# Kernel optimization log

Measured on AMD Instinct MI355X. Metric: run time of the kernel, lower is better.

Reference implementation:

```python
import jax, jax.numpy as jnp
import numpy as np

NUM_GLOBAL_EXPERTS = 256
LOCAL_START = 64  # global experts [64, 128) live on this rank


def setup_inputs() -> dict:
    key = jax.random.key(0)
    k1, = jax.random.split(key, 1)
    num_local_experts = 64
    # Routing ids: ~4.2M tokens x topk=8, values are GLOBAL expert ids in [0, 256)
    topk_ids = jax.random.randint(k1, (33554432,), 0, NUM_GLOBAL_EXPERTS, dtype=jnp.int32)
    # expert_map: global -> local; -1 for experts not owned by this rank
    gid = jnp.arange(NUM_GLOBAL_EXPERTS, dtype=jnp.int32)
    expert_map = jnp.where(
        (gid >= LOCAL_START) & (gid < LOCAL_START + num_local_experts),
        gid - LOCAL_START,
        jnp.int32(-1),
    )
    return {"topk_ids": topk_ids, "num_local_experts": num_local_experts, "expert_map": expert_map}


def reference(topk_ids, num_local_experts, expert_map=None):
    n = num_local_experts  # static python int
    ids = topk_ids.reshape(-1)
    if expert_map is not None:
        # invalid ids (< 0) stay invalid; valid global ids are remapped to local space
        ids = jnp.where(ids >= 0, expert_map[jnp.clip(ids, 0)], jnp.int32(-1))
    # Route all invalid / out-of-range ids into an overflow bucket n, then drop it.
    valid = (ids >= 0) & (ids < n)
    bucket = jnp.where(valid, ids, jnp.int32(n))
    counts = jax.ops.segment_sum(
        jnp.ones_like(bucket, dtype=jnp.int32), bucket, num_segments=n + 1
    )
    return counts[:n].astype(jnp.int32)
```

## Files before the change

### kernel.cpp

```cpp
#include <hip/hip_runtime.h>

#define BLOCK 256
#define NBLOCKS 1024
#define NBINS 256
#define NWAVES 4

__global__ __launch_bounds__(BLOCK) void hist_kernel(const int* __restrict__ ids,
                                                     int N,
                                                     const int* __restrict__ expert_map,
                                                     int* __restrict__ out,
                                                     int n_local) {
    __shared__ int lds[NWAVES * NBINS];
    const int tid = threadIdx.x;

    for (int i = tid; i < NWAVES * NBINS; i += BLOCK) lds[i] = 0;
    __syncthreads();

    int* h = &lds[(tid >> 6) * NBINS];

    const long long n4 = (long long)(N >> 2);
    const int4* __restrict__ ids4 = (const int4*)ids;
    const long long stride = (long long)gridDim.x * BLOCK;

    for (long long i = (long long)blockIdx.x * BLOCK + tid; i < n4; i += stride) {
        int4 v = ids4[i];
        atomicAdd(&h[v.x & (NBINS - 1)], 1);
        atomicAdd(&h[v.y & (NBINS - 1)], 1);
        atomicAdd(&h[v.z & (NBINS - 1)], 1);
        atomicAdd(&h[v.w & (NBINS - 1)], 1);
    }

    if (blockIdx.x == 0) {
        long long base = n4 << 2;
        for (long long i = base + tid; i < (long long)N; i += BLOCK) {
            atomicAdd(&h[ids[i] & (NBINS - 1)], 1);
        }
    }
    __syncthreads();

    if (tid < NBINS) {
        int sum = 0;
#pragma unroll
        for (int w = 0; w < NWAVES; ++w) sum += lds[w * NBINS + tid];
        int local = expert_map[tid];
        if (local >= 0 && local < n_local && sum > 0) {
            atomicAdd(&out[local], sum);
        }
    }
}

extern "C" void kernel_launch(void* const* d_in, const int* in_sizes, int n_in,
                              void* d_out, int out_size, void* d_ws, size_t ws_size,
                              hipStream_t stream) {
    const int* topk_ids = (const int*)d_in[0];
    const int* expert_map = (const int*)d_in[2];
    const int N = in_sizes[0];
    const int n_local = out_size;

    hipMemsetAsync(d_out, 0, (size_t)n_local * sizeof(int), stream);

    hist_kernel<<<NBLOCKS, BLOCK, 0, stream>>>(topk_ids, N, expert_map,
                                               (int*)d_out, n_local);
}
```

Measured before the change: 202.0 us.

## Split histogram into per-block partials plus reduction kernel, unroll loads

```diff
diff --git a/kernel.cpp b/kernel.cpp
--- a/kernel.cpp
+++ b/kernel.cpp
@@ -1,64 +1,98 @@
 #include <hip/hip_runtime.h>
 
-#define BLOCK 256
-#define NBLOCKS 1024
-#define NBINS 256
-#define NWAVES 4
+#define BLOCK   256
+#define NB1     2048
+#define NBINS   256
+#define NWAVES  (BLOCK / 64)
+#define UNROLL  4
 
-__global__ __launch_bounds__(BLOCK) void hist_kernel(const int* __restrict__ ids,
-                                                     int N,
-                                                     const int* __restrict__ expert_map,
-                                                     int* __restrict__ out,
-                                                     int n_local) {
+__global__ __launch_bounds__(BLOCK) void hist_part(const int* __restrict__ ids,
+                                                   int N,
+                                                   int* __restrict__ partials) {
     __shared__ int lds[NWAVES * NBINS];
     const int tid = threadIdx.x;
-
     for (int i = tid; i < NWAVES * NBINS; i += BLOCK) lds[i] = 0;
     __syncthreads();
 
     int* h = &lds[(tid >> 6) * NBINS];
 
-    const long long n4 = (long long)(N >> 2);
     const int4* __restrict__ ids4 = (const int4*)ids;
-    const long long stride = (long long)gridDim.x * BLOCK;
+    const int n4      = N >> 2;
+    const int chunk   = BLOCK * UNROLL;
+    const int gstride = (int)gridDim.x * chunk;
+    const int n4_full = (n4 / gstride) * gstride;
 
-    for (long long i = (long long)blockIdx.x * BLOCK + tid; i < n4; i += stride) {
+    for (int i = (int)blockIdx.x * chunk + tid; i < n4_full; i += gstride) {
+        int4 v[UNROLL];
+#pragma unroll
+        for (int u = 0; u < UNROLL; ++u) v[u] = ids4[i + u * BLOCK];
+#pragma unroll
+        for (int u = 0; u < UNROLL; ++u) {
+            atomicAdd(&h[v[u].x & (NBINS - 1)], 1);
+            atomicAdd(&h[v[u].y & (NBINS - 1)], 1);
+            atomicAdd(&h[v[u].z & (NBINS - 1)], 1);
+            atomicAdd(&h[v[u].w & (NBINS - 1)], 1);
+        }
+    }
+    for (int i = n4_full + (int)blockIdx.x * BLOCK + tid; i < n4;
+         i += (int)gridDim.x * BLOCK) {
         int4 v = ids4[i];
         atomicAdd(&h[v.x & (NBINS - 1)], 1);
         atomicAdd(&h[v.y & (NBINS - 1)], 1);
         atomicAdd(&h[v.z & (NBINS - 1)], 1);
         atomicAdd(&h[v.w & (NBINS - 1)], 1);
     }
-
     if (blockIdx.x == 0) {
-        long long base = n4 << 2;
-        for (long long i = base + tid; i < (long long)N; i += BLOCK) {
+        for (int i = (n4 << 2) + tid; i < N; i += BLOCK)
             atomicAdd(&h[ids[i] & (NBINS - 1)], 1);
-        }
     }
     __syncthreads();
 
-    if (tid < NBINS) {
-        int sum = 0;
+    for (int b = tid; b < NBINS; b += BLOCK) {
+        int s = 0;
 #pragma unroll
-        for (int w = 0; w < NWAVES; ++w) sum += lds[w * NBINS + tid];
-        int local = expert_map[tid];
-        if (local >= 0 && local < n_local && sum > 0) {
-            atomicAdd(&out[local], sum);
-        }
+        for (int w = 0; w < NWAVES; ++w) s += lds[w * NBINS + b];
+        partials[b * NB1 + blockIdx.x] = s;
+    }
+}
+
+__global__ __launch_bounds__(BLOCK) void reduce_part(const int* __restrict__ partials,
+                                                     const int* __restrict__ emap,
+                                                     int emap_n,
+                                                     int* __restrict__ out,
+                                                     int n_local) {
+    const int g = blockIdx.x;
+    const int tid = threadIdx.x;
+    int s = 0;
+    for (int j = tid; j < NB1; j += BLOCK) s += partials[g * NB1 + j];
+#pragma unroll
+    for (int off = 32; off > 0; off >>= 1) s += __shfl_down(s, off, 64);
+    __shared__ int wsum[NWAVES];
+    if ((tid & 63) == 0) wsum[tid >> 6] = s;
+    __syncthreads();
+    if (tid == 0) {
+        int tot = 0;
+#pragma unroll
+        for (int w = 0; w < NWAVES; ++w) tot += wsum[w];
+        int l = (g < emap_n) ? emap[g] : -1;
+        if ((unsigned)l < (unsigned)n_local && tot != 0) atomicAdd(&out[l], tot);
     }
 }
 
 extern "C" void kernel_launch(void* const* d_in, const int* in_sizes, int n_in,
                               void* d_out, int out_size, void* d_ws, size_t ws_size,
                               hipStream_t stream) {
-    const int* topk_ids = (const int*)d_in[0];
+    const int* topk_ids   = (const int*)d_in[0];
     const int* expert_map = (const int*)d_in[2];
-    const int N = in_sizes[0];
+    const int N       = in_sizes[0];
+    const int emap_n  = in_sizes[2];
     const int n_local = out_size;
+
+    int* partials = (int*)d_ws;
 
     hipMemsetAsync(d_out, 0, (size_t)n_local * sizeof(int), stream);
 
-    hist_kernel<<<NBLOCKS, BLOCK, 0, stream>>>(topk_ids, N, expert_map,
-                                               (int*)d_out, n_local);
+    hist_part<<<NB1, BLOCK, 0, stream>>>(topk_ids, N, partials);
+    reduce_part<<<NBINS, BLOCK, 0, stream>>>(partials, expert_map, emap_n,
+                                             (int*)d_out, n_local);
 }
```

Result: no change. 199.9 us (-1.1%).
